# Kernel optimization log

Measured on AMD Instinct MI355X. Metric: run time of the kernel, lower is better.

## Reference

```python
import jax, jax.numpy as jnp
import numpy as np

B = 8192
NV = 778   # MANO vertices
NJ = 16    # LBS joints
PARENTS = np.array([0, 0, 1, 2, 0, 4, 5, 0, 7, 8, 0, 10, 11, 0, 13, 14])


def quat2mat(quat):
    # quat: [N,4] (w,x,y,z) -> [N,3,3]
    q = quat / jnp.linalg.norm(quat, axis=1, keepdims=True)
    w, x, y, z = q[:, 0], q[:, 1], q[:, 2], q[:, 3]
    w2, x2, y2, z2 = w * w, x * x, y * y, z * z
    wx, wy, wz = w * x, w * y, w * z
    xy, xz, yz = x * y, x * z, y * z
    R = jnp.stack([
        w2 + x2 - y2 - z2, 2 * xy - 2 * wz, 2 * wy + 2 * xz,
        2 * wz + 2 * xy, w2 - x2 + y2 - z2, 2 * yz - 2 * wx,
        2 * xz - 2 * wy, 2 * wx + 2 * yz, w2 - x2 - y2 + z2,
    ], axis=1)
    return R.reshape(-1, 3, 3)


def batch_rodrigues(theta):
    # theta: [N,3] axis-angle -> [N,3,3]
    angle = jnp.linalg.norm(theta + 1e-8, axis=1, keepdims=True)
    normalized = theta / angle
    half = angle * 0.5
    quat = jnp.concatenate([jnp.cos(half), jnp.sin(half) * normalized], axis=1)
    return quat2mat(quat)


def qmul(q, r):
    # Hamilton product, (w,x,y,z); q,r: [N,4]
    w1, x1, y1, z1 = q[:, 0], q[:, 1], q[:, 2], q[:, 3]
    w2, x2, y2, z2 = r[:, 0], r[:, 1], r[:, 2], r[:, 3]
    return jnp.stack([
        w1 * w2 - x1 * x2 - y1 * y2 - z1 * z2,
        w1 * x2 + x1 * w2 + y1 * z2 - z1 * y2,
        w1 * y2 - x1 * z2 + y1 * w2 + z1 * x2,
        w1 * z2 + x1 * y2 - y1 * x2 + z1 * w2,
    ], axis=1)


def make_A(R, t):
    # R: [B,J,3,3], t: [B,J,3] -> [B,J,4,4]
    Bn, J = R.shape[0], R.shape[1]
    top = jnp.concatenate([R, t[..., None]], axis=-1)              # [B,J,3,4]
    bot = jnp.broadcast_to(jnp.array([0., 0., 0., 1.], R.dtype), (Bn, J, 1, 4))
    return jnp.concatenate([top, bot], axis=-2)


def mano_forward(theta, delta_quat, user_shape, init_quat, init_trans,
                 v_template, shapedirs, J_regressor, posedirs, weights):
    Bn = theta.shape[0]
    beta = jnp.broadcast_to(user_shape, (Bn, user_shape.shape[-1]))
    v_shaped = (beta @ shapedirs).reshape(Bn, NV, 3) + v_template   # [B,778,3]
    J = jnp.einsum('bvc,vj->bjc', v_shaped, J_regressor)            # [B,21,3]

    Rs = batch_rodrigues(theta.reshape(-1, 3)).reshape(Bn, 15, 3, 3)
    pose_feature = (Rs - jnp.eye(3, dtype=Rs.dtype)).reshape(Bn, 135)
    v_posed = (pose_feature @ posedirs).reshape(Bn, NV, 3) + v_shaped

    quat = qmul(delta_quat, jnp.broadcast_to(init_quat, (Bn, 4)))
    root_R = quat2mat(quat)                                          # [B,3,3]
    Rs_all = jnp.concatenate([root_R[:, None], Rs], axis=1)          # [B,16,3,3]

    Jk = J[:, :NJ]                                                   # [B,16,3]
    rel = Jk - Jk[:, PARENTS]
    rel = rel.at[:, 0].set(Jk[:, 0])                                 # root keeps absolute pos
    A_local = make_A(Rs_all, rel)                                    # [B,16,4,4]

    # kinematic chain (fixed 16-joint tree)
    results = [A_local[:, 0]]
    for i in range(1, NJ):
        results.append(results[PARENTS[i]] @ A_local[:, i])
    G = jnp.stack(results, axis=1)                                   # [B,16,4,4]

    Jw0 = jnp.concatenate([Jk, jnp.zeros((Bn, NJ, 1), Jk.dtype)], axis=-1)
    init_bone = jnp.einsum('bjkl,bjl->bjk', G, Jw0)                  # [B,16,4]
    A = jnp.concatenate([G[..., :3], G[..., 3:] - init_bone[..., None]], axis=-1)

    T = jnp.einsum('vj,bjkl->bvkl', weights, A)                      # [B,778,4,4]
    vp_homo = jnp.concatenate([v_posed, jnp.ones((Bn, NV, 1), v_posed.dtype)], axis=-1)
    verts = jnp.einsum('bvkl,bvl->bvk', T, vp_homo)[..., :3]         # [B,778,3]

    joints = jnp.einsum('bvc,vj->bjc', verts, J_regressor)           # [B,21,3]
    trans = init_trans.reshape(Bn, 1, 3)
    return joints + trans  # get_skin=False path


def setup_inputs() -> dict:
    key = jax.random.key(0)
    ks = jax.random.split(key, 10)
    return {
        'theta': jax.random.normal(ks[0], (B, 45), jnp.float32) * 0.3,
        'delta_quat': jax.random.normal(ks[1], (B, 4), jnp.float32),
        'user_shape': jax.random.normal(ks[2], (1, 10), jnp.float32),
        'init_quat': jax.random.normal(ks[3], (1, 4), jnp.float32),
        'init_trans': jax.random.normal(ks[4], (B, 3), jnp.float32),
        'v_template': jax.random.normal(ks[5], (NV, 3), jnp.float32),
        'shapedirs': jax.random.normal(ks[6], (10, NV * 3), jnp.float32) * 0.01,
        'J_regressor': jax.random.uniform(ks[7], (NV, 21), jnp.float32) / NV,
        'posedirs': jax.random.normal(ks[8], (135, NV * 3), jnp.float32) * 0.01,
        'weights': jax.random.uniform(ks[9], (NV, NJ), jnp.float32),
    }


def reference(theta, delta_quat, user_shape, init_quat, init_trans,
              v_template, shapedirs, J_regressor, posedirs, weights):
    return mano_forward(theta, delta_quat, user_shape, init_quat, init_trans,
                        v_template, shapedirs, J_regressor, posedirs, weights)
```

## Files before the change

kernel.cpp:

```cpp
#include <hip/hip_runtime.h>
#include <math.h>

#define B_SIZE 8192
#define NVERT 778
#define NP 135
#define NEC 416
#define KS16 16

#define OFF_JK    0
#define OFF_C1    64
#define OFF_C0    400
#define OFF_P2    1408
#define OFF_PFT   137488
#define OFF_AT    1243408
#define OFF_PP    137488
#define WS_END    2816272

__device__ inline void quat2mat_dev(float qw, float qx, float qy, float qz, float* R) {
  float n = sqrtf(qw*qw + qx*qx + qy*qy + qz*qz);
  float w = qw/n, x = qx/n, y = qy/n, z = qz/n;
  float w2=w*w, x2=x*x, y2=y*y, z2=z*z;
  float wx=w*x, wy=w*y, wz=w*z, xy=x*y, xz=x*z, yz=y*z;
  R[0]=w2+x2-y2-z2; R[1]=2.f*xy-2.f*wz; R[2]=2.f*wy+2.f*xz;
  R[3]=2.f*wz+2.f*xy; R[4]=w2-x2+y2-z2; R[5]=2.f*yz-2.f*wx;
  R[6]=2.f*xz-2.f*wy; R[7]=2.f*wx+2.f*yz; R[8]=w2-x2-y2+z2;
}

__device__ inline void rodrigues_dev(float tx, float ty, float tz, float* R) {
  float ax = tx + 1e-8f, ay = ty + 1e-8f, az = tz + 1e-8f;
  float angle = sqrtf(ax*ax + ay*ay + az*az);
  float nx = tx/angle, ny = ty/angle, nz = tz/angle;
  float half = 0.5f*angle;
  float cw = cosf(half), sw = sinf(half);
  quat2mat_dev(cw, sw*nx, sw*ny, sw*nz, R);
}

__global__ __launch_bounds__(256) void kA(const float* __restrict__ J_regressor,
                                          const float* __restrict__ weights,
                                          const float* __restrict__ posedirs,
                                          const float* __restrict__ user_shape,
                                          const float* __restrict__ v_template,
                                          const float* __restrict__ shapedirs,
                                          float* __restrict__ ws) {
  int tid = threadIdx.x;
  int bid = blockIdx.x;

  if (bid >= 416) {
    int j = bid - 416;
    __shared__ float red[3*256];
    __shared__ float ush[10];
    if (tid < 10) ush[tid] = user_shape[tid];
    __syncthreads();
    float p0 = 0.f, p1 = 0.f, p2 = 0.f;
    for (int v = tid; v < NVERT; v += 256) {
      float jr = J_regressor[v*21 + j];
      #pragma unroll
      for (int c = 0; c < 3; ++c) {
        int e = 3*v + c;
        float t = v_template[e];
        #pragma unroll
        for (int s = 0; s < 10; ++s) t += ush[s]*shapedirs[s*2334 + e];
        float val = jr * t;
        if (c == 0) p0 += val; else if (c == 1) p1 += val; else p2 += val;
      }
    }
    red[0*256+tid] = p0; red[1*256+tid] = p1; red[2*256+tid] = p2;
    __syncthreads();
    for (int s = 128; s > 0; s >>= 1) {
      if (tid < s) {
        red[0*256+tid] += red[0*256+tid+s];
        red[1*256+tid] += red[1*256+tid+s];
        red[2*256+tid] += red[2*256+tid+s];
      }
      __syncthreads();
    }
    if (tid < 3) ws[OFF_JK + j*3 + tid] = red[tid*256];
    return;
  }

  __shared__ float sJR[49*21];
  __shared__ float sW [49*16];
  __shared__ float sB [64*16];
  __shared__ float ush[10];
  if (tid < 10) ush[tid] = user_shape[tid];
  int ng = bid % 26;
  int ks = bid / 26;
  int vbeg = ks*49;
  int kt = min(NVERT - vbeg, 49);
  __syncthreads();
  for (int idx = tid; idx < kt*21; idx += 256) sJR[idx] = J_regressor[vbeg*21 + idx];
  for (int idx = tid; idx < kt*16; idx += 256) sW[idx]  = weights[vbeg*16 + idx];
  for (int idx = tid; idx < 16*64; idx += 256) {
    int s = idx >> 6, iv = idx & 63;
    if (iv < kt) {
      int ec = ng*16 + s;
      float val;
      if (ec > 408) val = 0.f;
      else if (ec == 408) val = 1.f;
      else {
        int c = ec / 136, pp = ec - c*136;
        int e = 3*(vbeg+iv) + c;
        if (pp == 135) {
          float t = v_template[e];
          #pragma unroll
          for (int s0 = 0; s0 < 10; ++s0) t += ush[s0]*shapedirs[s0*2334 + e];
          val = t;
        } else {
          val = posedirs[pp*2334 + e];
        }
      }
      sB[iv*16 + s] = val;
    }
  }
  __syncthreads();
  if (tid < 168) {
    int cg2 = (tid < 84) ? 0 : 1;
    int r4  = (tid < 84) ? tid : tid - 84;
    int q2 = 4*r4;
    int j2 = q2 >> 4;
    int jb = q2 & 15;
    float acc[4][8];
    #pragma unroll
    for (int r = 0; r < 4; ++r)
      #pragma unroll
      for (int s = 0; s < 8; ++s) acc[r][s] = 0.f;
    for (int i = 0; i < kt; ++i) {
      float jr = sJR[i*21 + j2];
      float4 w4 = *(const float4*)&sW[i*16 + jb];
      float4 b0 = *(const float4*)&sB[i*16 + cg2*8];
      float4 b1 = *(const float4*)&sB[i*16 + cg2*8 + 4];
      float wv[4] = {w4.x, w4.y, w4.z, w4.w};
      #pragma unroll
      for (int r = 0; r < 4; ++r) {
        float s2 = jr * wv[r];
        acc[r][0] += s2*b0.x; acc[r][1] += s2*b0.y;
        acc[r][2] += s2*b0.z; acc[r][3] += s2*b0.w;
        acc[r][4] += s2*b1.x; acc[r][5] += s2*b1.y;
        acc[r][6] += s2*b1.z; acc[r][7] += s2*b1.w;
      }
    }
    float* Pp = ws + OFF_PP + (size_t)ks*NEC*336;
    #pragma unroll
    for (int s = 0; s < 8; ++s) {
      int ec = ng*16 + cg2*8 + s;
      float4 v4 = make_float4(acc[0][s], acc[1][s], acc[2][s], acc[3][s]);
      *(float4*)&Pp[ec*336 + q2] = v4;
    }
  }
}

__global__ void kR(float* __restrict__ ws) {
  int idx = blockIdx.x*256 + threadIdx.x;
  if (idx >= 416*84) return;
  int ec = idx / 84, q4 = idx - ec*84;
  const float* Pp = ws + OFF_PP;
  float4 s = make_float4(0.f, 0.f, 0.f, 0.f);
  #pragma unroll
  for (int ks = 0; ks < KS16; ++ks) {
    float4 v = *(const float4*)&Pp[(size_t)ks*NEC*336 + ec*336 + 4*q4];
    s.x += v.x; s.y += v.y; s.z += v.z; s.w += v.w;
  }
  float sv[4] = {s.x, s.y, s.z, s.w};
  #pragma unroll
  for (int r = 0; r < 4; ++r) {
    int q2 = 4*q4 + r;
    int jj2 = q2 >> 4, jj = q2 & 15;
    if (ec < 408) {
      int c = ec / 136, pp = ec - c*136;
      if (pp < 135) ws[OFF_P2 + (size_t)(jj2*135 + pp)*48 + jj*3 + c] = sv[r];
      else          ws[OFF_C0 + jj2*48 + jj*3 + c] = sv[r];
    } else if (ec == 408) {
      ws[OFF_C1 + jj2*16 + jj] = sv[r];
    }
  }
}

__global__ __launch_bounds__(256) void k4_pose(const float* __restrict__ theta,
                                               const float* __restrict__ delta_quat,
                                               const float* __restrict__ init_quat,
                                               float* __restrict__ ws) {
  int bid = blockIdx.x;
  int u  = bid % 6;
  int bb = bid / 6;
  int b  = bb*256 + threadIdx.x;
  __shared__ float jk[48], rel[48];
  if (threadIdx.x < 48) {
    float v = ws[OFF_JK + threadIdx.x];
    jk[threadIdx.x] = v;
    int j = threadIdx.x/3, c = threadIdx.x - j*3;
    float r;
    if (j == 0) r = v;
    else {
      int par = (((j-1) % 3) == 0) ? 0 : (j-1);
      r = v - ws[OFF_JK + par*3 + c];
    }
    rel[threadIdx.x] = r;
  }
  __syncthreads();
  float* pfT = ws + OFF_PFT;
  float* AT  = ws + OFF_AT;

  float w1=delta_quat[b*4+0], x1=delta_quat[b*4+1], y1=delta_quat[b*4+2], z1=delta_quat[b*4+3];
  float w2=init_quat[0], x2=init_quat[1], y2=init_quat[2], z2=init_quat[3];
  float qw = w1*w2 - x1*x2 - y1*y2 - z1*z2;
  float qx = w1*x2 + x1*w2 + y1*z2 - z1*y2;
  float qy = w1*y2 - x1*z2 + y1*w2 + z1*x2;
  float qz = w1*z2 + x1*y2 - y1*x2 + z1*w2;
  float G[12];
  quat2mat_dev(qw, qx, qy, qz, G);
  G[9] = rel[0]; G[10] = rel[1]; G[11] = rel[2];

  if (u == 5) {
    #pragma unroll
    for (int c = 0; c < 3; ++c) {
      float g0 = G[c*3+0], g1 = G[c*3+1], g2 = G[c*3+2];
      AT[(size_t)(c*4+0)*B_SIZE + b] = g0;
      AT[(size_t)(c*4+1)*B_SIZE + b] = g1;
      AT[(size_t)(c*4+2)*B_SIZE + b] = g2;
      AT[(size_t)(c*4+3)*B_SIZE + b] = G[9+c] - (g0*jk[0] + g1*jk[1] + g2*jk[2]);
    }
    return;
  }

  #pragma unroll
  for (int mstep = 0; mstep < 3; ++mstep) {
    int j = 3*u + 1 + mstep;
    int i = j - 1;
    float R[9];
    rodrigues_dev(theta[b*45+3*i+0], theta[b*45+3*i+1], theta[b*45+3*i+2], R);
    pfT[(size_t)(9*i+0)*B_SIZE + b] = R[0]-1.f;
    pfT[(size_t)(9*i+1)*B_SIZE + b] = R[1];
    pfT[(size_t)(9*i+2)*B_SIZE + b] = R[2];
    pfT[(size_t)(9*i+3)*B_SIZE + b] = R[3];
    pfT[(size_t)(9*i+4)*B_SIZE + b] = R[4]-1.f;
    pfT[(size_t)(9*i+5)*B_SIZE + b] = R[5];
    pfT[(size_t)(9*i+6)*B_SIZE + b] = R[6];
    pfT[(size_t)(9*i+7)*B_SIZE + b] = R[7];
    pfT[(size_t)(9*i+8)*B_SIZE + b] = R[8]-1.f;
    float nG[12];
    const float* rj = rel + j*3;
    #pragma unroll
    for (int r3 = 0; r3 < 3; ++r3) {
      float a0 = G[r3*3+0], a1 = G[r3*3+1], a2 = G[r3*3+2];
      nG[r3*3+0] = a0*R[0] + a1*R[3] + a2*R[6];
      nG[r3*3+1] = a0*R[1] + a1*R[4] + a2*R[7];
      nG[r3*3+2] = a0*R[2] + a1*R[5] + a2*R[8];
      nG[9+r3]   = G[9+r3] + a0*rj[0] + a1*rj[1] + a2*rj[2];
    }
    #pragma unroll
    for (int k = 0; k < 12; ++k) G[k] = nG[k];
    const float* jkj = jk + j*3;
    #pragma unroll
    for (int c = 0; c < 3; ++c) {
      float g0 = G[c*3+0], g1 = G[c*3+1], g2 = G[c*3+2];
      AT[(size_t)(j*12 + c*4+0)*B_SIZE + b] = g0;
      AT[(size_t)(j*12 + c*4+1)*B_SIZE + b] = g1;
      AT[(size_t)(j*12 + c*4+2)*B_SIZE + b] = g2;
      AT[(size_t)(j*12 + c*4+3)*B_SIZE + b] = G[9+c] - (g0*jkj[0] + g1*jkj[1] + g2*jkj[2]);
    }
  }
}

__global__ __launch_bounds__(256) void k5_main(const float* __restrict__ init_trans,
                                               const float* __restrict__ ws,
                                               float* __restrict__ out) {
  __shared__ int s_voff[1];
  int g = blockIdx.x;
  int xcd = g & 7, k = g >> 3;
  int br  = ((k & 3) << 3) | xcd;
  int j2  = k >> 2;
  int tid = threadIdx.x;
  int b   = br*256 + tid;

  if (tid == 0) s_voff[0] = j2*135*12;
  __syncthreads();
  int voff = s_voff[0];

  float4 acc[12];
  const float4* c04 = (const float4*)(ws + OFF_C0 + j2*48);
  #pragma unroll
  for (int i = 0; i < 12; ++i) acc[i] = c04[i];

  const float* pfT = ws + OFF_PFT;
  const float4* P24 = (const float4*)(ws + OFF_P2) + voff;
  #pragma unroll 3
  for (int p = 0; p < NP; ++p) {
    float pf = pfT[(size_t)p*B_SIZE + b];
    const float4* Pr = P24 + p*12;
    #pragma unroll
    for (int i = 0; i < 12; ++i) {
      float4 pv = Pr[i];
      acc[i].x += pf*pv.x; acc[i].y += pf*pv.y;
      acc[i].z += pf*pv.z; acc[i].w += pf*pv.w;
    }
  }

  float m[48];
  #pragma unroll
  for (int i = 0; i < 12; ++i) {
    m[4*i+0] = acc[i].x; m[4*i+1] = acc[i].y;
    m[4*i+2] = acc[i].z; m[4*i+3] = acc[i].w;
  }

  const float* AT  = ws + OFF_AT;
  const float* c1p = ws + OFF_C1 + j2*16;
  float o0 = 0.f, o1 = 0.f, o2 = 0.f;
  #pragma unroll
  for (int j = 0; j < 16; ++j) {
    float c1 = c1p[j];
    float m0 = m[3*j+0], m1 = m[3*j+1], m2 = m[3*j+2];
    #pragma unroll
    for (int k2 = 0; k2 < 3; ++k2) {
      float a0 = AT[(size_t)(j*12 + k2*4+0)*B_SIZE + b];
      float a1 = AT[(size_t)(j*12 + k2*4+1)*B_SIZE + b];
      float a2 = AT[(size_t)(j*12 + k2*4+2)*B_SIZE + b];
      float a3 = AT[(size_t)(j*12 + k2*4+3)*B_SIZE + b];
      float r = a0*m0 + a1*m1 + a2*m2 + a3*c1;
      if (k2 == 0) o0 += r; else if (k2 == 1) o1 += r; else o2 += r;
    }
  }
  size_t ob = ((size_t)b*21 + j2)*3;
  out[ob+0] = o0 + init_trans[b*3+0];
  out[ob+1] = o1 + init_trans[b*3+1];
  out[ob+2] = o2 + init_trans[b*3+2];
}

extern "C" void kernel_launch(void* const* d_in, const int* in_sizes, int n_in,
                              void* d_out, int out_size, void* d_ws, size_t ws_size,
                              hipStream_t stream) {
  const float* theta       = (const float*)d_in[0];
  const float* delta_quat  = (const float*)d_in[1];
  const float* user_shape  = (const float*)d_in[2];
  const float* init_quat   = (const float*)d_in[3];
  const float* init_trans  = (const float*)d_in[4];
  const float* v_template  = (const float*)d_in[5];
  const float* shapedirs   = (const float*)d_in[6];
  const float* J_regressor = (const float*)d_in[7];
  const float* posedirs    = (const float*)d_in[8];
  const float* weights     = (const float*)d_in[9];
  float* out = (float*)d_out;
  float* ws  = (float*)d_ws;

  kA<<<432, 256, 0, stream>>>(J_regressor, weights, posedirs,
                              user_shape, v_template, shapedirs, ws);
  kR<<<137, 256, 0, stream>>>(ws);
  k4_pose<<<192, 256, 0, stream>>>(theta, delta_quat, init_quat, ws);
  k5_main<<<672, 256, 0, stream>>>(init_trans, ws, out);
}
```

Baseline: 142.2 us.

## Fuse pose kernel into main kernel, recomputing rotations per thread

Removes the separate pose kernel, which wrote rotation features and per-joint transforms to global workspace. The main kernel now recomputes Rodrigues rotations and the kinematic chain per thread, and folds the joint offset algebraically into the accumulated terms. This drops a launch and the global write/read traffic for pfT and AT. In exchange each of the 21 j2 blocks per batch row redoes the trig and chain math twice, and the loops are no longer unrolled, which may cost registers and ALU time.

Result: slower. 170.4 us (+19.9%).

```diff
diff --git a/kernel.cpp b/kernel.cpp
--- a/kernel.cpp
+++ b/kernel.cpp
@@ -11,10 +11,8 @@
 #define OFF_C1    64
 #define OFF_C0    400
 #define OFF_P2    1408
-#define OFF_PFT   137488
-#define OFF_AT    1243408
 #define OFF_PP    137488
-#define WS_END    2816272
+#define WS_END    2373904
 
 __device__ inline void quat2mat_dev(float qw, float qx, float qy, float qz, float* R) {
   float n = sqrtf(qw*qw + qx*qx + qy*qy + qz*qz);
@@ -175,95 +173,13 @@
   }
 }
 
-__global__ __launch_bounds__(256) void k4_pose(const float* __restrict__ theta,
-                                               const float* __restrict__ delta_quat,
-                                               const float* __restrict__ init_quat,
-                                               float* __restrict__ ws) {
-  int bid = blockIdx.x;
-  int u  = bid % 6;
-  int bb = bid / 6;
-  int b  = bb*256 + threadIdx.x;
-  __shared__ float jk[48], rel[48];
-  if (threadIdx.x < 48) {
-    float v = ws[OFF_JK + threadIdx.x];
-    jk[threadIdx.x] = v;
-    int j = threadIdx.x/3, c = threadIdx.x - j*3;
-    float r;
-    if (j == 0) r = v;
-    else {
-      int par = (((j-1) % 3) == 0) ? 0 : (j-1);
-      r = v - ws[OFF_JK + par*3 + c];
-    }
-    rel[threadIdx.x] = r;
-  }
-  __syncthreads();
-  float* pfT = ws + OFF_PFT;
-  float* AT  = ws + OFF_AT;
-
-  float w1=delta_quat[b*4+0], x1=delta_quat[b*4+1], y1=delta_quat[b*4+2], z1=delta_quat[b*4+3];
-  float w2=init_quat[0], x2=init_quat[1], y2=init_quat[2], z2=init_quat[3];
-  float qw = w1*w2 - x1*x2 - y1*y2 - z1*z2;
-  float qx = w1*x2 + x1*w2 + y1*z2 - z1*y2;
-  float qy = w1*y2 - x1*z2 + y1*w2 + z1*x2;
-  float qz = w1*z2 + x1*y2 - y1*x2 + z1*w2;
-  float G[12];
-  quat2mat_dev(qw, qx, qy, qz, G);
-  G[9] = rel[0]; G[10] = rel[1]; G[11] = rel[2];
-
-  if (u == 5) {
-    #pragma unroll
-    for (int c = 0; c < 3; ++c) {
-      float g0 = G[c*3+0], g1 = G[c*3+1], g2 = G[c*3+2];
-      AT[(size_t)(c*4+0)*B_SIZE + b] = g0;
-      AT[(size_t)(c*4+1)*B_SIZE + b] = g1;
-      AT[(size_t)(c*4+2)*B_SIZE + b] = g2;
-      AT[(size_t)(c*4+3)*B_SIZE + b] = G[9+c] - (g0*jk[0] + g1*jk[1] + g2*jk[2]);
-    }
-    return;
-  }
-
-  #pragma unroll
-  for (int mstep = 0; mstep < 3; ++mstep) {
-    int j = 3*u + 1 + mstep;
-    int i = j - 1;
-    float R[9];
-    rodrigues_dev(theta[b*45+3*i+0], theta[b*45+3*i+1], theta[b*45+3*i+2], R);
-    pfT[(size_t)(9*i+0)*B_SIZE + b] = R[0]-1.f;
-    pfT[(size_t)(9*i+1)*B_SIZE + b] = R[1];
-    pfT[(size_t)(9*i+2)*B_SIZE + b] = R[2];
-    pfT[(size_t)(9*i+3)*B_SIZE + b] = R[3];
-    pfT[(size_t)(9*i+4)*B_SIZE + b] = R[4]-1.f;
-    pfT[(size_t)(9*i+5)*B_SIZE + b] = R[5];
-    pfT[(size_t)(9*i+6)*B_SIZE + b] = R[6];
-    pfT[(size_t)(9*i+7)*B_SIZE + b] = R[7];
-    pfT[(size_t)(9*i+8)*B_SIZE + b] = R[8]-1.f;
-    float nG[12];
-    const float* rj = rel + j*3;
-    #pragma unroll
-    for (int r3 = 0; r3 < 3; ++r3) {
-      float a0 = G[r3*3+0], a1 = G[r3*3+1], a2 = G[r3*3+2];
-      nG[r3*3+0] = a0*R[0] + a1*R[3] + a2*R[6];
-      nG[r3*3+1] = a0*R[1] + a1*R[4] + a2*R[7];
-      nG[r3*3+2] = a0*R[2] + a1*R[5] + a2*R[8];
-      nG[9+r3]   = G[9+r3] + a0*rj[0] + a1*rj[1] + a2*rj[2];
-    }
-    #pragma unroll
-    for (int k = 0; k < 12; ++k) G[k] = nG[k];
-    const float* jkj = jk + j*3;
-    #pragma unroll
-    for (int c = 0; c < 3; ++c) {
-      float g0 = G[c*3+0], g1 = G[c*3+1], g2 = G[c*3+2];
-      AT[(size_t)(j*12 + c*4+0)*B_SIZE + b] = g0;
-      AT[(size_t)(j*12 + c*4+1)*B_SIZE + b] = g1;
-      AT[(size_t)(j*12 + c*4+2)*B_SIZE + b] = g2;
-      AT[(size_t)(j*12 + c*4+3)*B_SIZE + b] = G[9+c] - (g0*jkj[0] + g1*jkj[1] + g2*jkj[2]);
-    }
-  }
-}
-
-__global__ __launch_bounds__(256) void k5_main(const float* __restrict__ init_trans,
-                                               const float* __restrict__ ws,
-                                               float* __restrict__ out) {
+__global__ __launch_bounds__(256) void k5f(const float* __restrict__ theta,
+                                           const float* __restrict__ delta_quat,
+                                           const float* __restrict__ init_quat,
+                                           const float* __restrict__ init_trans,
+                                           const float* __restrict__ ws,
+                                           float* __restrict__ out) {
+  __shared__ float s_jk[48], s_rel[48];
   __shared__ int s_voff[1];
   int g = blockIdx.x;
   int xcd = g & 7, k = g >> 3;
@@ -273,50 +189,98 @@
   int b   = br*256 + tid;
 
   if (tid == 0) s_voff[0] = j2*135*12;
+  if (tid < 48) {
+    float v = ws[OFF_JK + tid];
+    s_jk[tid] = v;
+    int j = tid/3, c = tid - j*3;
+    float r;
+    if (j == 0) r = v;
+    else {
+      int par = (((j-1) % 3) == 0) ? 0 : (j-1);
+      r = v - ws[OFF_JK + par*3 + c];
+    }
+    s_rel[tid] = r;
+  }
   __syncthreads();
   int voff = s_voff[0];
 
-  float4 acc[12];
-  const float4* c04 = (const float4*)(ws + OFF_C0 + j2*48);
-  #pragma unroll
-  for (int i = 0; i < 12; ++i) acc[i] = c04[i];
-
-  const float* pfT = ws + OFF_PFT;
+  float m[48];
+  {
+    const float* C0r = ws + OFF_C0 + j2*48;
+    #pragma unroll
+    for (int i = 0; i < 48; ++i) m[i] = C0r[i];
+  }
+
+  const float* th = theta + (size_t)b*45;
   const float4* P24 = (const float4*)(ws + OFF_P2) + voff;
-  #pragma unroll 3
-  for (int p = 0; p < NP; ++p) {
-    float pf = pfT[(size_t)p*B_SIZE + b];
-    const float4* Pr = P24 + p*12;
-    #pragma unroll
-    for (int i = 0; i < 12; ++i) {
-      float4 pv = Pr[i];
-      acc[i].x += pf*pv.x; acc[i].y += pf*pv.y;
-      acc[i].z += pf*pv.z; acc[i].w += pf*pv.w;
-    }
-  }
-
-  float m[48];
-  #pragma unroll
-  for (int i = 0; i < 12; ++i) {
-    m[4*i+0] = acc[i].x; m[4*i+1] = acc[i].y;
-    m[4*i+2] = acc[i].z; m[4*i+3] = acc[i].w;
-  }
-
-  const float* AT  = ws + OFF_AT;
+
+  for (int i = 0; i < 15; ++i) {
+    float R[9];
+    rodrigues_dev(th[3*i+0], th[3*i+1], th[3*i+2], R);
+    float pf[9] = {R[0]-1.f, R[1], R[2], R[3], R[4]-1.f, R[5], R[6], R[7], R[8]-1.f};
+    const float4* Pi = P24 + i*9*12;
+    #pragma unroll
+    for (int r = 0; r < 9; ++r) {
+      float s = pf[r];
+      const float4* Pr = Pi + r*12;
+      #pragma unroll
+      for (int kk = 0; kk < 12; ++kk) {
+        float4 pv = Pr[kk];
+        m[4*kk+0] += s*pv.x; m[4*kk+1] += s*pv.y;
+        m[4*kk+2] += s*pv.z; m[4*kk+3] += s*pv.w;
+      }
+    }
+  }
+
   const float* c1p = ws + OFF_C1 + j2*16;
   float o0 = 0.f, o1 = 0.f, o2 = 0.f;
-  #pragma unroll
-  for (int j = 0; j < 16; ++j) {
-    float c1 = c1p[j];
-    float m0 = m[3*j+0], m1 = m[3*j+1], m2 = m[3*j+2];
-    #pragma unroll
-    for (int k2 = 0; k2 < 3; ++k2) {
-      float a0 = AT[(size_t)(j*12 + k2*4+0)*B_SIZE + b];
-      float a1 = AT[(size_t)(j*12 + k2*4+1)*B_SIZE + b];
-      float a2 = AT[(size_t)(j*12 + k2*4+2)*B_SIZE + b];
-      float a3 = AT[(size_t)(j*12 + k2*4+3)*B_SIZE + b];
-      float r = a0*m0 + a1*m1 + a2*m2 + a3*c1;
-      if (k2 == 0) o0 += r; else if (k2 == 1) o1 += r; else o2 += r;
+
+  float Gr[12];
+  {
+    float w1=delta_quat[b*4+0], x1=delta_quat[b*4+1], y1=delta_quat[b*4+2], z1=delta_quat[b*4+3];
+    float w2=init_quat[0], x2=init_quat[1], y2=init_quat[2], z2=init_quat[3];
+    float qw = w1*w2 - x1*x2 - y1*y2 - z1*z2;
+    float qx = w1*x2 + x1*w2 + y1*z2 - z1*y2;
+    float qy = w1*y2 - x1*z2 + y1*w2 + z1*x2;
+    float qz = w1*z2 + x1*y2 - y1*x2 + z1*w2;
+    quat2mat_dev(qw, qx, qy, qz, Gr);
+    Gr[9] = s_rel[0]; Gr[10] = s_rel[1]; Gr[11] = s_rel[2];
+  }
+  {
+    float c1 = c1p[0];
+    float t0 = m[0] - c1*s_jk[0], t1 = m[1] - c1*s_jk[1], t2 = m[2] - c1*s_jk[2];
+    o0 += Gr[0]*t0 + Gr[1]*t1 + Gr[2]*t2 + Gr[9]*c1;
+    o1 += Gr[3]*t0 + Gr[4]*t1 + Gr[5]*t2 + Gr[10]*c1;
+    o2 += Gr[6]*t0 + Gr[7]*t1 + Gr[8]*t2 + Gr[11]*c1;
+  }
+  for (int u = 0; u < 5; ++u) {
+    float G[12];
+    #pragma unroll
+    for (int q = 0; q < 12; ++q) G[q] = Gr[q];
+    for (int ms = 0; ms < 3; ++ms) {
+      int j = 3*u + 1 + ms;
+      int i = j - 1;
+      float R[9];
+      rodrigues_dev(th[3*i+0], th[3*i+1], th[3*i+2], R);
+      float nG[12];
+      const float* rj = s_rel + j*3;
+      #pragma unroll
+      for (int r3 = 0; r3 < 3; ++r3) {
+        float a0 = G[r3*3+0], a1 = G[r3*3+1], a2 = G[r3*3+2];
+        nG[r3*3+0] = a0*R[0] + a1*R[3] + a2*R[6];
+        nG[r3*3+1] = a0*R[1] + a1*R[4] + a2*R[7];
+        nG[r3*3+2] = a0*R[2] + a1*R[5] + a2*R[8];
+        nG[9+r3]   = G[9+r3] + a0*rj[0] + a1*rj[1] + a2*rj[2];
+      }
+      #pragma unroll
+      for (int q = 0; q < 12; ++q) G[q] = nG[q];
+      float c1 = c1p[j];
+      const float* jk3 = s_jk + j*3;
+      float m0 = m[3*j+0], m1 = m[3*j+1], m2 = m[3*j+2];
+      float t0 = m0 - c1*jk3[0], t1 = m1 - c1*jk3[1], t2 = m2 - c1*jk3[2];
+      o0 += G[0]*t0 + G[1]*t1 + G[2]*t2 + G[9]*c1;
+      o1 += G[3]*t0 + G[4]*t1 + G[5]*t2 + G[10]*c1;
+      o2 += G[6]*t0 + G[7]*t1 + G[8]*t2 + G[11]*c1;
     }
   }
   size_t ob = ((size_t)b*21 + j2)*3;
@@ -344,6 +308,5 @@
   kA<<<432, 256, 0, stream>>>(J_regressor, weights, posedirs,
                               user_shape, v_template, shapedirs, ws);
   kR<<<137, 256, 0, stream>>>(ws);
-  k4_pose<<<192, 256, 0, stream>>>(theta, delta_quat, init_quat, ws);
-  k5_main<<<672, 256, 0, stream>>>(init_trans, ws, out);
-}
+  k5f<<<672, 256, 0, stream>>>(theta, delta_quat, init_quat, init_trans, ws, out);
+}
```
